# Kernel tuning notes

Measured on AMD Instinct MI355X. Metric: run time of the kernel, lower is better.

## Reference

```python
import jax, jax.numpy as jnp
import numpy as np

D_MODEL = 1024
N_EXPERTS = 8
D_FF = 4096
B, S = 2, 2048
INIT_SCALE = 0.02


def setup_inputs() -> dict:
    key = jax.random.key(0)
    ks = jax.random.split(key, 8)
    x = jax.random.normal(ks[0], (B, S, D_MODEL), dtype=jnp.float32)
    gate_w = jax.random.normal(ks[1], (D_MODEL, N_EXPERTS), dtype=jnp.float32) * INIT_SCALE
    gate_b = jnp.zeros((N_EXPERTS,), dtype=jnp.float32)
    w1 = jax.random.normal(ks[2], (N_EXPERTS, D_MODEL, D_FF), dtype=jnp.float32) * INIT_SCALE
    b1 = jnp.zeros((N_EXPERTS, D_FF), dtype=jnp.float32)
    w2 = jax.random.normal(ks[3], (N_EXPERTS, D_FF, D_MODEL), dtype=jnp.float32) * INIT_SCALE
    b2 = jnp.zeros((N_EXPERTS, D_MODEL), dtype=jnp.float32)
    return {"x": x, "gate_w": gate_w, "gate_b": gate_b,
            "w1": w1, "b1": b1, "w2": w2, "b2": b2}


def reference(x, gate_w, gate_b, w1, b1, w2, b2):
    E = w1.shape[0]
    # --- Top2Router ---
    logits = x @ gate_w + gate_b                      # [B,S,E]
    scores = jax.nn.softmax(logits, axis=-1)          # [B,S,E]
    val, idx = jax.lax.top_k(scores, 2)               # [B,S,2]
    # scatter top-2 softmax values into a dense [B,S,E] dispatch mask
    dispatch = (jax.nn.one_hot(idx, E, dtype=scores.dtype) * val[..., None]).sum(axis=-2)
    expert_counts = dispatch.sum(axis=(0, 1))         # [E]
    # --- dense loop over experts (vectorized over E), masked combine ---
    # h: [B,E,S,d_ff]
    h = jax.nn.gelu(jnp.einsum('bsd,edf->besf', x, w1) + b1[None, :, None, :],
                    approximate=False)
    y = jnp.einsum('besf,efd->besd', h, w2) + b2[None, :, None, :]  # [B,E,S,D]
    out = jnp.einsum('besd,bse->bsd', y, dispatch)    # masked sum over experts
    return out, dispatch, expert_counts
```

## Files before the change

kernel.cpp:

```cpp
#include <hip/hip_runtime.h>
#include <hip/hip_bf16.h>
#include <math.h>

#define DM    1024
#define NE    8
#define DF    4096
#define NT    4096
#define RCAP  9216
#define OUT_N   (NT*DM)
#define DISP_N  (NT*NE)
#define TOTAL_OUT (OUT_N + DISP_N + NE)

typedef __attribute__((ext_vector_type(4))) float f32x4;
typedef __attribute__((ext_vector_type(8))) short bf16x8;

#define WS_CNT    0
#define WS_FILL   32
#define WS_OFFS   64
#define WS_TOK    128
#define WS_WGT    (WS_TOK + RCAP*4)
#define WS_TOPE   (WS_WGT + RCAP*4)
#define WS_TOPV   (WS_TOPE + NT*2*4)
#define WS_W1T    (((WS_TOPV + NT*2*4) + 255) & ~255ul)
#define WS_W2T    (WS_W1T + (size_t)NE*DF*DM*2)
#define WS_XG     (WS_W2T + (size_t)NE*DM*DF*2)
#define WS_H      (WS_XG  + (size_t)RCAP*DM*2)

__device__ __forceinline__ void async_copy16(const __hip_bfloat16* g, __hip_bfloat16* l) {
    __builtin_amdgcn_global_load_lds(
        (const __attribute__((address_space(1))) unsigned int*)g,
        (__attribute__((address_space(3))) unsigned int*)l, 16, 0, 0);
}

__global__ void init_kernel(float* __restrict__ out, int* __restrict__ cnt,
                            int* __restrict__ fill, int* __restrict__ tok) {
    int gid = blockIdx.x * blockDim.x + threadIdx.x;
    int stride = gridDim.x * blockDim.x;
    for (int i = gid; i < TOTAL_OUT; i += stride) out[i] = 0.0f;
    if (gid < RCAP) tok[gid] = -1;
    if (gid < NE) { cnt[gid] = 0; fill[gid] = 0; }
}

__global__ void transpose_cast(const float* __restrict__ in, __hip_bfloat16* __restrict__ outp,
                               int R, int C) {
    __shared__ float tile[32][33];
    int e = blockIdx.z;
    int c0 = blockIdx.x * 32, r0 = blockIdx.y * 32;
    const float* ib = in + (size_t)e * R * C;
    __hip_bfloat16* ob = outp + (size_t)e * R * C;
    int tx = threadIdx.x & 31, ty = threadIdx.x >> 5;
    for (int rr = ty; rr < 32; rr += 8)
        tile[rr][tx] = ib[(size_t)(r0 + rr) * C + c0 + tx];
    __syncthreads();
    for (int cc = ty; cc < 32; cc += 8)
        ob[(size_t)(c0 + cc) * R + r0 + tx] = __float2bfloat16(tile[tx][cc]);
}

__global__ void gate_kernel(const float* __restrict__ x, const float* __restrict__ gw,
                            const float* __restrict__ gb, float* __restrict__ disp,
                            float* __restrict__ counts, int* __restrict__ cnt,
                            int* __restrict__ tope, float* __restrict__ topv) {
    int t = blockIdx.x;
    int l = threadIdx.x;
    const float* xr = x + (size_t)t * DM;
    double p[NE];
    #pragma unroll
    for (int e = 0; e < NE; ++e) p[e] = 0.0;
    for (int i = 0; i < DM / 64; ++i) {
        int d = l + 64 * i;
        double xv = (double)xr[d];
        const float* gr = gw + (size_t)d * NE;
        #pragma unroll
        for (int e = 0; e < NE; ++e) p[e] += xv * (double)gr[e];
    }
    #pragma unroll
    for (int off = 32; off > 0; off >>= 1) {
        #pragma unroll
        for (int e = 0; e < NE; ++e) p[e] += __shfl_xor(p[e], off, 64);
    }
    if (l == 0) {
        double lg[NE];
        double m = -1e300;
        #pragma unroll
        for (int e = 0; e < NE; ++e) { lg[e] = p[e] + (double)gb[e]; m = fmax(m, lg[e]); }
        double s = 0.0;
        #pragma unroll
        for (int e = 0; e < NE; ++e) s += exp(lg[e] - m);
        int e1 = 0;
        #pragma unroll
        for (int e = 1; e < NE; ++e) if (lg[e] > lg[e1]) e1 = e;
        int e2 = (e1 == 0) ? 1 : 0;
        #pragma unroll
        for (int e = 0; e < NE; ++e) if (e != e1 && lg[e] > lg[e2]) e2 = e;
        float v1 = (float)(exp(lg[e1] - m) / s);
        float v2 = (float)(exp(lg[e2] - m) / s);
        float* dr = disp + (size_t)t * NE;
        #pragma unroll
        for (int e = 0; e < NE; ++e) dr[e] = 0.0f;
        dr[e1] = v1; dr[e2] = v2;
        atomicAdd(&counts[e1], v1);
        atomicAdd(&counts[e2], v2);
        atomicAdd(&cnt[e1], 1);
        atomicAdd(&cnt[e2], 1);
        tope[2 * t] = e1;     topv[2 * t] = v1;
        tope[2 * t + 1] = e2; topv[2 * t + 1] = v2;
    }
}

__global__ void scan_kernel(const int* __restrict__ cnt, int* __restrict__ offs) {
    if (threadIdx.x == 0 && blockIdx.x == 0) {
        int o = 0;
        for (int e = 0; e < NE; ++e) {
            offs[e] = o;
            o += (cnt[e] + 127) & ~127;
        }
        offs[NE] = o;
    }
}

__global__ void build_kernel(const int* __restrict__ tope, const float* __restrict__ topv,
                             const int* __restrict__ offs, int* __restrict__ fill,
                             int* __restrict__ tok, float* __restrict__ wgt) {
    int t = blockIdx.x * blockDim.x + threadIdx.x;
    if (t >= NT) return;
    #pragma unroll
    for (int s = 0; s < 2; ++s) {
        int e = tope[2 * t + s];
        int pos = atomicAdd(&fill[e], 1);
        int row = offs[e] + pos;
        tok[row] = t;
        wgt[row] = topv[2 * t + s];
    }
}

__global__ void gather_kernel(const float* __restrict__ x, const int* __restrict__ tok,
                              __hip_bfloat16* __restrict__ xg) {
    int row = blockIdx.x;
    int t = tok[row];
    if (t < 0) return;
    int i = threadIdx.x;
    const float4 v = ((const float4*)(x + (size_t)t * DM))[i];
    ushort4 o;
    o.x = __bfloat16_as_ushort(__float2bfloat16(v.x));
    o.y = __bfloat16_as_ushort(__float2bfloat16(v.y));
    o.z = __bfloat16_as_ushort(__float2bfloat16(v.z));
    o.w = __bfloat16_as_ushort(__float2bfloat16(v.w));
    ((ushort4*)(xg + (size_t)row * DM))[i] = o;
}


__global__ __launch_bounds__(256) void gemm1_kernel(
    const __hip_bfloat16* __restrict__ xg, const __hip_bfloat16* __restrict__ w1t,
    const float* __restrict__ b1, __hip_bfloat16* __restrict__ h,
    const int* __restrict__ offs, const int* __restrict__ cnt) {
    __shared__ __hip_bfloat16 As[128 * 32];
    __shared__ __hip_bfloat16 Bs[128 * 32];
    const int row0 = blockIdx.y * 128;
    const int total = offs[NE];
    if (row0 >= total) return;
    int e = 0;
    while (row0 >= offs[e + 1]) ++e;
    if (row0 >= offs[e] + cnt[e]) return;
    const int n0 = blockIdx.x * 128;
    const __hip_bfloat16* Ab = xg + (size_t)row0 * DM;
    const __hip_bfloat16* Bb = w1t + (size_t)e * DF * DM + (size_t)n0 * DM;

    const int tid = threadIdx.x, lane = tid & 63, wave = tid >> 6;
    const int wm = wave >> 1, wn = wave & 1, g = lane >> 4, r = lane & 15;
    const int c1 = tid, c2 = tid + 256;

    f32x4 acc[4][4];
    #pragma unroll
    for (int m = 0; m < 4; ++m)
        #pragma unroll
        for (int n = 0; n < 4; ++n)
            #pragma unroll
            for (int j = 0; j < 4; ++j) acc[m][n][j] = 0.0f;

    for (int k0 = 0; k0 < DM; k0 += 32) {
        async_copy16(Ab + (size_t)(c1 >> 2) * DM + k0 + (c1 & 3) * 8, As + c1 * 8);
        async_copy16(Ab + (size_t)(c2 >> 2) * DM + k0 + (c2 & 3) * 8, As + c2 * 8);
        async_copy16(Bb + (size_t)(c1 >> 2) * DM + k0 + (c1 & 3) * 8, Bs + c1 * 8);
        async_copy16(Bb + (size_t)(c2 >> 2) * DM + k0 + (c2 & 3) * 8, Bs + c2 * 8);
        __syncthreads();
        bf16x8 af[4], bfr[4];
        #pragma unroll
        for (int m = 0; m < 4; ++m)
            af[m] = *(const bf16x8*)(As + (wm * 64 + m * 16 + r) * 32 + g * 8);
        #pragma unroll
        for (int n = 0; n < 4; ++n)
            bfr[n] = *(const bf16x8*)(Bs + (wn * 64 + n * 16 + r) * 32 + g * 8);
        #pragma unroll
        for (int m = 0; m < 4; ++m)
            #pragma unroll
            for (int n = 0; n < 4; ++n)
                acc[m][n] = __builtin_amdgcn_mfma_f32_16x16x32_bf16(af[m], bfr[n], acc[m][n], 0, 0, 0);
        __syncthreads();
    }
    float bb[4];
    #pragma unroll
    for (int n = 0; n < 4; ++n) bb[n] = b1[(size_t)e * DF + n0 + wn * 64 + n * 16 + r];
    #pragma unroll
    for (int m = 0; m < 4; ++m) {
        #pragma unroll
        for (int i = 0; i < 4; ++i) {
            int rowi = row0 + wm * 64 + m * 16 + g * 4 + i;
            __hip_bfloat16* hr = h + (size_t)rowi * DF + n0 + wn * 64 + r;
            #pragma unroll
            for (int n = 0; n < 4; ++n) {
                float v = acc[m][n][i] + bb[n];
                float ge = 0.5f * v * (1.0f + erff(v * 0.70710678118654752f));
                hr[n * 16] = __float2bfloat16(ge);
            }
        }
    }
}

__global__ __launch_bounds__(256) void gemm2_kernel(
    const __hip_bfloat16* __restrict__ h, const __hip_bfloat16* __restrict__ w2t,
    const float* __restrict__ b2, float* __restrict__ out,
    const int* __restrict__ offs, const int* __restrict__ cnt,
    const int* __restrict__ tok, const float* __restrict__ wgt) {
    __shared__ __hip_bfloat16 As[128 * 32];
    __shared__ __hip_bfloat16 Bs[128 * 32];
    const int row0 = blockIdx.y * 128;
    const int total = offs[NE];
    if (row0 >= total) return;
    int e = 0;
    while (row0 >= offs[e + 1]) ++e;
    if (row0 >= offs[e] + cnt[e]) return;
    const int n0 = blockIdx.x * 128;
    const __hip_bfloat16* Ab = h + (size_t)row0 * DF;
    const __hip_bfloat16* Bb = w2t + (size_t)e * DM * DF + (size_t)n0 * DF;

    const int tid = threadIdx.x, lane = tid & 63, wave = tid >> 6;
    const int wm = wave >> 1, wn = wave & 1, g = lane >> 4, r = lane & 15;
    const int c1 = tid, c2 = tid + 256;

    f32x4 acc[4][4];
    #pragma unroll
    for (int m = 0; m < 4; ++m)
        #pragma unroll
        for (int n = 0; n < 4; ++n)
            #pragma unroll
            for (int j = 0; j < 4; ++j) acc[m][n][j] = 0.0f;

    for (int k0 = 0; k0 < DF; k0 += 32) {
        async_copy16(Ab + (size_t)(c1 >> 2) * DF + k0 + (c1 & 3) * 8, As + c1 * 8);
        async_copy16(Ab + (size_t)(c2 >> 2) * DF + k0 + (c2 & 3) * 8, As + c2 * 8);
        async_copy16(Bb + (size_t)(c1 >> 2) * DF + k0 + (c1 & 3) * 8, Bs + c1 * 8);
        async_copy16(Bb + (size_t)(c2 >> 2) * DF + k0 + (c2 & 3) * 8, Bs + c2 * 8);
        __syncthreads();
        bf16x8 af[4], bfr[4];
        #pragma unroll
        for (int m = 0; m < 4; ++m)
            af[m] = *(const bf16x8*)(As + (wm * 64 + m * 16 + r) * 32 + g * 8);
        #pragma unroll
        for (int n = 0; n < 4; ++n)
            bfr[n] = *(const bf16x8*)(Bs + (wn * 64 + n * 16 + r) * 32 + g * 8);
        #pragma unroll
        for (int m = 0; m < 4; ++m)
            #pragma unroll
            for (int n = 0; n < 4; ++n)
                acc[m][n] = __builtin_amdgcn_mfma_f32_16x16x32_bf16(af[m], bfr[n], acc[m][n], 0, 0, 0);
        __syncthreads();
    }
    float bb[4];
    #pragma unroll
    for (int n = 0; n < 4; ++n) bb[n] = b2[(size_t)e * DM + n0 + wn * 64 + n * 16 + r];
    #pragma unroll
    for (int m = 0; m < 4; ++m) {
        #pragma unroll
        for (int i = 0; i < 4; ++i) {
            int rowi = row0 + wm * 64 + m * 16 + g * 4 + i;
            int t = tok[rowi];
            if (t < 0) continue;
            float wv = wgt[rowi];
            float* orow = out + (size_t)t * DM + n0 + wn * 64 + r;
            #pragma unroll
            for (int n = 0; n < 4; ++n)
                atomicAdd(orow + n * 16, wv * (acc[m][n][i] + bb[n]));
        }
    }
}

extern "C" void kernel_launch(void* const* d_in, const int* in_sizes, int n_in,
                              void* d_out, int out_size, void* d_ws, size_t ws_size,
                              hipStream_t stream) {
    const float* x  = (const float*)d_in[0];
    const float* gw = (const float*)d_in[1];
    const float* gb = (const float*)d_in[2];
    const float* w1 = (const float*)d_in[3];
    const float* b1 = (const float*)d_in[4];
    const float* w2 = (const float*)d_in[5];
    const float* b2 = (const float*)d_in[6];

    float* out    = (float*)d_out;
    float* disp   = out + OUT_N;
    float* counts = disp + DISP_N;

    char* ws = (char*)d_ws;
    int*   cnt  = (int*)(ws + WS_CNT);
    int*   fill = (int*)(ws + WS_FILL);
    int*   offs = (int*)(ws + WS_OFFS);
    int*   tok  = (int*)(ws + WS_TOK);
    float* wgt  = (float*)(ws + WS_WGT);
    int*   tope = (int*)(ws + WS_TOPE);
    float* topv = (float*)(ws + WS_TOPV);
    __hip_bfloat16* w1t = (__hip_bfloat16*)(ws + WS_W1T);
    __hip_bfloat16* w2t = (__hip_bfloat16*)(ws + WS_W2T);
    __hip_bfloat16* xg  = (__hip_bfloat16*)(ws + WS_XG);
    __hip_bfloat16* h   = (__hip_bfloat16*)(ws + WS_H);

    init_kernel<<<4096, 256, 0, stream>>>(out, cnt, fill, tok);
    transpose_cast<<<dim3(DF / 32, DM / 32, NE), 256, 0, stream>>>(w1, w1t, DM, DF);
    transpose_cast<<<dim3(DM / 32, DF / 32, NE), 256, 0, stream>>>(w2, w2t, DF, DM);
    gate_kernel<<<NT, 64, 0, stream>>>(x, gw, gb, disp, counts, cnt, tope, topv);
    scan_kernel<<<1, 64, 0, stream>>>(cnt, offs);
    build_kernel<<<NT / 256, 256, 0, stream>>>(tope, topv, offs, fill, tok, wgt);
    gather_kernel<<<RCAP, 256, 0, stream>>>(x, tok, xg);
    gemm1_kernel<<<dim3(DF / 128, RCAP / 128), 256, 0, stream>>>(xg, w1t, b1, h, offs, cnt);
    gemm2_kernel<<<dim3(DM / 128, RCAP / 128), 256, 0, stream>>>(h, w2t, b2, out, offs, cnt, tok, wgt);
}
```

Measured before the change: 786.0 us.

## Widen GEMM K-tile to 64 with XOR-swizzled LDS, XCD-aware grid remap, vectorized transpose

```diff
diff --git a/kernel.cpp b/kernel.cpp
--- a/kernel.cpp
+++ b/kernel.cpp
@@ -41,19 +41,30 @@
     if (gid < NE) { cnt[gid] = 0; fill[gid] = 0; }
 }
 
-__global__ void transpose_cast(const float* __restrict__ in, __hip_bfloat16* __restrict__ outp,
-                               int R, int C) {
-    __shared__ float tile[32][33];
+__global__ __launch_bounds__(256) void transpose_cast2(const float* __restrict__ in,
+                                                       __hip_bfloat16* __restrict__ outp,
+                                                       int R, int C) {
+    __shared__ ushort tile[64][72];
     int e = blockIdx.z;
-    int c0 = blockIdx.x * 32, r0 = blockIdx.y * 32;
+    int c0 = blockIdx.x * 64, r0 = blockIdx.y * 64;
     const float* ib = in + (size_t)e * R * C;
-    __hip_bfloat16* ob = outp + (size_t)e * R * C;
-    int tx = threadIdx.x & 31, ty = threadIdx.x >> 5;
-    for (int rr = ty; rr < 32; rr += 8)
-        tile[rr][tx] = ib[(size_t)(r0 + rr) * C + c0 + tx];
+    ushort* ob = (ushort*)outp + (size_t)e * R * C;
+    int tx = threadIdx.x & 15, ty = threadIdx.x >> 4;
+    #pragma unroll
+    for (int j = 0; j < 4; ++j) {
+        int row = ty + 16 * j;
+        float4 v = *(const float4*)(ib + (size_t)(r0 + row) * C + c0 + tx * 4);
+        tile[tx * 4 + 0][row] = __bfloat16_as_ushort(__float2bfloat16(v.x));
+        tile[tx * 4 + 1][row] = __bfloat16_as_ushort(__float2bfloat16(v.y));
+        tile[tx * 4 + 2][row] = __bfloat16_as_ushort(__float2bfloat16(v.z));
+        tile[tx * 4 + 3][row] = __bfloat16_as_ushort(__float2bfloat16(v.w));
+    }
     __syncthreads();
-    for (int cc = ty; cc < 32; cc += 8)
-        ob[(size_t)(c0 + cc) * R + r0 + tx] = __float2bfloat16(tile[tx][cc]);
+    #pragma unroll
+    for (int j = 0; j < 4; ++j) {
+        int cc = ty + 16 * j;
+        *(ushort4*)(ob + (size_t)(c0 + cc) * R + r0 + tx * 4) = *(const ushort4*)&tile[cc][tx * 4];
+    }
 }
 
 __global__ void gate_kernel(const float* __restrict__ x, const float* __restrict__ gw,
@@ -153,21 +164,41 @@
     const __hip_bfloat16* __restrict__ xg, const __hip_bfloat16* __restrict__ w1t,
     const float* __restrict__ b1, __hip_bfloat16* __restrict__ h,
     const int* __restrict__ offs, const int* __restrict__ cnt) {
-    __shared__ __hip_bfloat16 As[128 * 32];
-    __shared__ __hip_bfloat16 Bs[128 * 32];
-    const int row0 = blockIdx.y * 128;
+    __shared__ __attribute__((aligned(128))) __hip_bfloat16 As[128 * 64];
+    __shared__ __attribute__((aligned(128))) __hip_bfloat16 Bs[128 * 64];
+    const int NXT = DF / 128;
+    const int nwg = NXT * (RCAP / 128);
+    int wg = (int)blockIdx.x;
+    int id = (wg & 7) * (nwg >> 3) + (wg >> 3);
+    const int bx = id % NXT, by = id / NXT;
+    const int row0 = by * 128;
     const int total = offs[NE];
     if (row0 >= total) return;
     int e = 0;
     while (row0 >= offs[e + 1]) ++e;
     if (row0 >= offs[e] + cnt[e]) return;
-    const int n0 = blockIdx.x * 128;
+    const int n0 = bx * 128;
     const __hip_bfloat16* Ab = xg + (size_t)row0 * DM;
     const __hip_bfloat16* Bb = w1t + (size_t)e * DF * DM + (size_t)n0 * DM;
 
     const int tid = threadIdx.x, lane = tid & 63, wave = tid >> 6;
     const int wm = wave >> 1, wn = wave & 1, g = lane >> 4, r = lane & 15;
-    const int c1 = tid, c2 = tid + 256;
+    const int rr = lane >> 3;
+    const int kx = (((lane & 7) ^ rr) << 3);
+    size_t soff[4]; int doff[4];
+    #pragma unroll
+    for (int qi = 0; qi < 4; ++qi) {
+        int q = wave * 4 + qi;
+        soff[qi] = (size_t)(q * 8 + rr) * DM + kx;
+        doff[qi] = q * 512 + lane * 8;
+    }
+    int rowA[4], rowB[4], tsw[2];
+    #pragma unroll
+    for (int m = 0; m < 4; ++m) rowA[m] = (wm * 64 + m * 16 + r) * 64;
+    #pragma unroll
+    for (int n = 0; n < 4; ++n) rowB[n] = (wn * 64 + n * 16 + r) * 64;
+    tsw[0] = ((g ^ (r & 7)) << 3);
+    tsw[1] = (((4 + g) ^ (r & 7)) << 3);
 
     f32x4 acc[4][4];
     #pragma unroll
@@ -177,24 +208,26 @@
             #pragma unroll
             for (int j = 0; j < 4; ++j) acc[m][n][j] = 0.0f;
 
-    for (int k0 = 0; k0 < DM; k0 += 32) {
-        async_copy16(Ab + (size_t)(c1 >> 2) * DM + k0 + (c1 & 3) * 8, As + c1 * 8);
-        async_copy16(Ab + (size_t)(c2 >> 2) * DM + k0 + (c2 & 3) * 8, As + c2 * 8);
-        async_copy16(Bb + (size_t)(c1 >> 2) * DM + k0 + (c1 & 3) * 8, Bs + c1 * 8);
-        async_copy16(Bb + (size_t)(c2 >> 2) * DM + k0 + (c2 & 3) * 8, Bs + c2 * 8);
+    for (int k0 = 0; k0 < DM; k0 += 64) {
+        #pragma unroll
+        for (int qi = 0; qi < 4; ++qi) {
+            async_copy16(Ab + soff[qi] + k0, As + doff[qi]);
+            async_copy16(Bb + soff[qi] + k0, Bs + doff[qi]);
+        }
         __syncthreads();
-        bf16x8 af[4], bfr[4];
-        #pragma unroll
-        for (int m = 0; m < 4; ++m)
-            af[m] = *(const bf16x8*)(As + (wm * 64 + m * 16 + r) * 32 + g * 8);
-        #pragma unroll
-        for (int n = 0; n < 4; ++n)
-            bfr[n] = *(const bf16x8*)(Bs + (wn * 64 + n * 16 + r) * 32 + g * 8);
-        #pragma unroll
-        for (int m = 0; m < 4; ++m)
-            #pragma unroll
-            for (int n = 0; n < 4; ++n)
-                acc[m][n] = __builtin_amdgcn_mfma_f32_16x16x32_bf16(af[m], bfr[n], acc[m][n], 0, 0, 0);
+        #pragma unroll
+        for (int hh = 0; hh < 2; ++hh) {
+            bf16x8 af[4], bfr[4];
+            #pragma unroll
+            for (int m = 0; m < 4; ++m) af[m] = *(const bf16x8*)(As + rowA[m] + tsw[hh]);
+            #pragma unroll
+            for (int n = 0; n < 4; ++n) bfr[n] = *(const bf16x8*)(Bs + rowB[n] + tsw[hh]);
+            #pragma unroll
+            for (int m = 0; m < 4; ++m)
+                #pragma unroll
+                for (int n = 0; n < 4; ++n)
+                    acc[m][n] = __builtin_amdgcn_mfma_f32_16x16x32_bf16(af[m], bfr[n], acc[m][n], 0, 0, 0);
+        }
         __syncthreads();
     }
     float bb[4];
@@ -221,21 +254,41 @@
     const float* __restrict__ b2, float* __restrict__ out,
     const int* __restrict__ offs, const int* __restrict__ cnt,
     const int* __restrict__ tok, const float* __restrict__ wgt) {
-    __shared__ __hip_bfloat16 As[128 * 32];
-    __shared__ __hip_bfloat16 Bs[128 * 32];
-    const int row0 = blockIdx.y * 128;
+    __shared__ __attribute__((aligned(128))) __hip_bfloat16 As[128 * 64];
+    __shared__ __attribute__((aligned(128))) __hip_bfloat16 Bs[128 * 64];
+    const int NXT = DM / 128;
+    const int nwg = NXT * (RCAP / 128);
+    int wg = (int)blockIdx.x;
+    int id = (wg & 7) * (nwg >> 3) + (wg >> 3);
+    const int bx = id % NXT, by = id / NXT;
+    const int row0 = by * 128;
     const int total = offs[NE];
     if (row0 >= total) return;
     int e = 0;
     while (row0 >= offs[e + 1]) ++e;
     if (row0 >= offs[e] + cnt[e]) return;
-    const int n0 = blockIdx.x * 128;
+    const int n0 = bx * 128;
     const __hip_bfloat16* Ab = h + (size_t)row0 * DF;
     const __hip_bfloat16* Bb = w2t + (size_t)e * DM * DF + (size_t)n0 * DF;
 
     const int tid = threadIdx.x, lane = tid & 63, wave = tid >> 6;
     const int wm = wave >> 1, wn = wave & 1, g = lane >> 4, r = lane & 15;
-    const int c1 = tid, c2 = tid + 256;
+    const int rr = lane >> 3;
+    const int kx = (((lane & 7) ^ rr) << 3);
+    size_t soff[4]; int doff[4];
+    #pragma unroll
+    for (int qi = 0; qi < 4; ++qi) {
+        int q = wave * 4 + qi;
+        soff[qi] = (size_t)(q * 8 + rr) * DF + kx;
+        doff[qi] = q * 512 + lane * 8;
+    }
+    int rowA[4], rowB[4], tsw[2];
+    #pragma unroll
+    for (int m = 0; m < 4; ++m) rowA[m] = (wm * 64 + m * 16 + r) * 64;
+    #pragma unroll
+    for (int n = 0; n < 4; ++n) rowB[n] = (wn * 64 + n * 16 + r) * 64;
+    tsw[0] = ((g ^ (r & 7)) << 3);
+    tsw[1] = (((4 + g) ^ (r & 7)) << 3);
 
     f32x4 acc[4][4];
     #pragma unroll
@@ -245,24 +298,26 @@
             #pragma unroll
             for (int j = 0; j < 4; ++j) acc[m][n][j] = 0.0f;
 
-    for (int k0 = 0; k0 < DF; k0 += 32) {
-        async_copy16(Ab + (size_t)(c1 >> 2) * DF + k0 + (c1 & 3) * 8, As + c1 * 8);
-        async_copy16(Ab + (size_t)(c2 >> 2) * DF + k0 + (c2 & 3) * 8, As + c2 * 8);
-        async_copy16(Bb + (size_t)(c1 >> 2) * DF + k0 + (c1 & 3) * 8, Bs + c1 * 8);
-        async_copy16(Bb + (size_t)(c2 >> 2) * DF + k0 + (c2 & 3) * 8, Bs + c2 * 8);
+    for (int k0 = 0; k0 < DF; k0 += 64) {
+        #pragma unroll
+        for (int qi = 0; qi < 4; ++qi) {
+            async_copy16(Ab + soff[qi] + k0, As + doff[qi]);
+            async_copy16(Bb + soff[qi] + k0, Bs + doff[qi]);
+        }
         __syncthreads();
-        bf16x8 af[4], bfr[4];
-        #pragma unroll
-        for (int m = 0; m < 4; ++m)
-            af[m] = *(const bf16x8*)(As + (wm * 64 + m * 16 + r) * 32 + g * 8);
-        #pragma unroll
-        for (int n = 0; n < 4; ++n)
-            bfr[n] = *(const bf16x8*)(Bs + (wn * 64 + n * 16 + r) * 32 + g * 8);
-        #pragma unroll
-        for (int m = 0; m < 4; ++m)
-            #pragma unroll
-            for (int n = 0; n < 4; ++n)
-                acc[m][n] = __builtin_amdgcn_mfma_f32_16x16x32_bf16(af[m], bfr[n], acc[m][n], 0, 0, 0);
+        #pragma unroll
+        for (int hh = 0; hh < 2; ++hh) {
+            bf16x8 af[4], bfr[4];
+            #pragma unroll
+            for (int m = 0; m < 4; ++m) af[m] = *(const bf16x8*)(As + rowA[m] + tsw[hh]);
+            #pragma unroll
+            for (int n = 0; n < 4; ++n) bfr[n] = *(const bf16x8*)(Bs + rowB[n] + tsw[hh]);
+            #pragma unroll
+            for (int m = 0; m < 4; ++m)
+                #pragma unroll
+                for (int n = 0; n < 4; ++n)
+                    acc[m][n] = __builtin_amdgcn_mfma_f32_16x16x32_bf16(af[m], bfr[n], acc[m][n], 0, 0, 0);
+        }
         __syncthreads();
     }
     float bb[4];
@@ -313,12 +368,12 @@
     __hip_bfloat16* h   = (__hip_bfloat16*)(ws + WS_H);
 
     init_kernel<<<4096, 256, 0, stream>>>(out, cnt, fill, tok);
-    transpose_cast<<<dim3(DF / 32, DM / 32, NE), 256, 0, stream>>>(w1, w1t, DM, DF);
-    transpose_cast<<<dim3(DM / 32, DF / 32, NE), 256, 0, stream>>>(w2, w2t, DF, DM);
+    transpose_cast2<<<dim3(DF / 64, DM / 64, NE), 256, 0, stream>>>(w1, w1t, DM, DF);
+    transpose_cast2<<<dim3(DM / 64, DF / 64, NE), 256, 0, stream>>>(w2, w2t, DF, DM);
     gate_kernel<<<NT, 64, 0, stream>>>(x, gw, gb, disp, counts, cnt, tope, topv);
     scan_kernel<<<1, 64, 0, stream>>>(cnt, offs);
     build_kernel<<<NT / 256, 256, 0, stream>>>(tope, topv, offs, fill, tok, wgt);
     gather_kernel<<<RCAP, 256, 0, stream>>>(x, tok, xg);
-    gemm1_kernel<<<dim3(DF / 128, RCAP / 128), 256, 0, stream>>>(xg, w1t, b1, h, offs, cnt);
-    gemm2_kernel<<<dim3(DM / 128, RCAP / 128), 256, 0, stream>>>(h, w2t, b2, out, offs, cnt, tok, wgt);
-}
+    gemm1_kernel<<<(DF / 128) * (RCAP / 128), 256, 0, stream>>>(xg, w1t, b1, h, offs, cnt);
+    gemm2_kernel<<<(DM / 128) * (RCAP / 128), 256, 0, stream>>>(h, w2t, b2, out, offs, cnt, tok, wgt);
+}
```

New measurement: 815.6 us. 3.8% more time.
